# Kernel optimization log

Hardware: AMD Instinct MI355X
Metric: run time of the kernel (lower is better)

## Reference

```python
import jax, jax.numpy as jnp
import numpy as np
import math

HIDDEN = 1024
HEADS = 16
HEAD_DIM = HIDDEN // HEADS


def setup_inputs() -> dict:
    key = jax.random.key(0)
    k1, k2, k3, k4, k5 = jax.random.split(key, 5)
    B, S = 2, 2048
    scale = 1.0 / math.sqrt(HIDDEN)
    return {
        "batch_hidden": jax.random.normal(k1, (B, S, HIDDEN), dtype=jnp.float32),
        # nn.Linear weights are [out, in]; y = x @ W.T
        "Wq": jax.random.uniform(k2, (HIDDEN, HIDDEN), jnp.float32, -scale, scale),
        "Wk": jax.random.uniform(k3, (HIDDEN, HIDDEN), jnp.float32, -scale, scale),
        "Wg": jax.random.uniform(k4, (HIDDEN, HIDDEN), jnp.float32, -scale, scale),
        "bg": jax.random.uniform(k5, (HIDDEN,), jnp.float32, -scale, scale),
    }


def _split_heads(x):
    # [B,S,H] -> [B,heads,S,head_dim]
    B, S, _ = x.shape
    return x.reshape(B, S, HEADS, HEAD_DIM).transpose(0, 2, 1, 3)


def reference(batch_hidden, Wq, Wk, Wg, bg):
    # NOTE: faithful to source — value uses the KEY projection weights.
    q = batch_hidden @ Wq.T
    k = batch_hidden @ Wk.T
    v = batch_hidden @ Wk.T
    gate = jax.nn.sigmoid(batch_hidden @ Wg.T + bg)  # [B,S,H]

    q = _split_heads(q)  # [B,h,S,d]
    k = _split_heads(k)
    v = _split_heads(v)

    # source: scores = K @ Q^T (softmax over query positions)
    scores = jnp.einsum("bhkd,bhqd->bhkq", k, q) / math.sqrt(HEAD_DIM)
    attn = jax.nn.softmax(scores, axis=-1)  # [B,h,S,S]

    ctx = jnp.einsum("bhkq,bhqd->bhkd", attn, v)  # [B,h,S,d]
    ctx = ctx.transpose(0, 2, 1, 3).reshape(batch_hidden.shape)  # [B,S,H]

    out = gate * ctx
    return out, attn
```

## Files before the change

kernel.cpp:

```cpp
#include <hip/hip_runtime.h>
#include <hip/hip_bf16.h>

#define HID 1024
#define NHEADS 16
#define HDIM 64
#define SEQ 2048
#define NTOK 4096

typedef __attribute__((ext_vector_type(8))) short short8;
typedef __attribute__((ext_vector_type(4))) float f32x4;
typedef unsigned short ush;

__device__ __forceinline__ ush f2bf(float f) {
    unsigned int u = __float_as_uint(f);
    u = (u + 0x7fffu + ((u >> 16) & 1u)) >> 16;
    return (ush)u;
}
__device__ __forceinline__ void async_copy16(const void* g, void* l) {
    __builtin_amdgcn_global_load_lds(
        (const __attribute__((address_space(1))) void*)g,
        (__attribute__((address_space(3))) void*)l, 16, 0, 0);
}
#define SBAR()  __builtin_amdgcn_s_barrier()
#define SCHED() __builtin_amdgcn_sched_barrier(0)

__global__ __launch_bounds__(256) void cvt_kernel(
    const float* __restrict__ X, const float* __restrict__ Wq,
    const float* __restrict__ Wk, const float* __restrict__ Wg,
    ush* __restrict__ Xbf, ush* __restrict__ Wbf)
{
    long i = (long)blockIdx.x * 256 + threadIdx.x;
    const float* src; ush* dst; long j;
    if (i < 524288)      { src = X;  dst = Xbf;           j = i; }
    else if (i < 655360) { src = Wq; dst = Wbf;           j = i - 524288; }
    else if (i < 786432) { src = Wk; dst = Wbf + 1048576; j = i - 655360; }
    else                 { src = Wg; dst = Wbf + 2097152; j = i - 786432; }
    float4 a = *reinterpret_cast<const float4*>(src + j * 8);
    float4 b = *reinterpret_cast<const float4*>(src + j * 8 + 4);
    short8 o;
    o[0] = (short)f2bf(a.x); o[1] = (short)f2bf(a.y);
    o[2] = (short)f2bf(a.z); o[3] = (short)f2bf(a.w);
    o[4] = (short)f2bf(b.x); o[5] = (short)f2bf(b.y);
    o[6] = (short)f2bf(b.z); o[7] = (short)f2bf(b.w);
    *reinterpret_cast<short8*>(dst + j * 8) = o;
}

__global__ __launch_bounds__(256, 2) void proj_kernel(
    const ush* __restrict__ Xbf, const ush* __restrict__ Wbf,
    const float* __restrict__ bgp,
    ush* __restrict__ Qbf, ush* __restrict__ Kbf,
    float* __restrict__ gate)
{
    __shared__ __align__(16) ush As[2][128 * 64];
    __shared__ __align__(16) ush Bs[2][128 * 64];

    const int lin = blockIdx.y * 24 + blockIdx.x;
    const int swz = (lin & 7) * 96 + (lin >> 3);
    const int n0 = (swz % 24) * 128;
    const int m0 = (swz / 24) * 128;
    const int tid = threadIdx.x, lane = tid & 63, wv = tid >> 6;
    const int wm = wv >> 1, wn = wv & 1;
    const int l16 = lane & 15, lq = lane >> 4;
    const int lrow = lane >> 3, lc = lane & 7;
    const int scU = lc ^ lrow;
    const int u0 = lq ^ (l16 & 7);

    f32x4 acc[4][4];
    #pragma unroll
    for (int i = 0; i < 4; i++)
        #pragma unroll
        for (int j = 0; j < 4; j++)
            #pragma unroll
            for (int r = 0; r < 4; r++) acc[i][j][r] = 0.0f;

    const ush* gA = Xbf + (long)m0 * HID;
    const ush* gB = Wbf + (long)n0 * HID;

    auto stage = [&](int k0, int bu) {
        #pragma unroll
        for (int c = 0; c < 4; ++c) {
            int chunk = wv * 4 + c;
            int row = chunk * 8 + lrow;
            async_copy16(gA + (long)row * HID + k0 + scU * 8, &As[bu][chunk * 512]);
            async_copy16(gB + (long)row * HID + k0 + scU * 8, &Bs[bu][chunk * 512]);
        }
    };

    stage(0, 0);
    stage(64, 1);

    for (int k = 0; k < 16; ++k) {
        const int cur = k & 1;
        if (k == 15) asm volatile("s_waitcnt vmcnt(0)" ::: "memory");
        else         asm volatile("s_waitcnt vmcnt(8)" ::: "memory");
        SCHED();
        SBAR(); SCHED();
        #pragma unroll
        for (int ks = 0; ks < 2; ++ks) {
            const int uo = (ks ? (u0 ^ 4) : u0) * 8;
            short8 a[4], b[4];
            #pragma unroll
            for (int mf = 0; mf < 4; mf++)
                a[mf] = *reinterpret_cast<const short8*>(&As[cur][(wm * 64 + mf * 16 + l16) * 64 + uo]);
            #pragma unroll
            for (int nf = 0; nf < 4; nf++)
                b[nf] = *reinterpret_cast<const short8*>(&Bs[cur][(wn * 64 + nf * 16 + l16) * 64 + uo]);
            #pragma unroll
            for (int mf = 0; mf < 4; mf++)
                #pragma unroll
                for (int nf = 0; nf < 4; nf++)
                    acc[mf][nf] = __builtin_amdgcn_mfma_f32_16x16x32_bf16(a[mf], b[nf], acc[mf][nf], 0, 0, 0);
        }
        SBAR(); SCHED();
        if (k < 14) stage((k + 2) * 64, cur);
    }

    const int z = n0 >> 10;
    #pragma unroll
    for (int mf = 0; mf < 4; mf++)
        #pragma unroll
        for (int nf = 0; nf < 4; nf++) {
            int row = m0 + wm * 64 + mf * 16 + lq * 4;
            int col = (n0 + wn * 64 + nf * 16 + l16) & 1023;
            #pragma unroll
            for (int r = 0; r < 4; r++) {
                float v = acc[mf][nf][r];
                long idx = (long)(row + r) * HID + col;
                if (z == 0)      Qbf[idx] = f2bf(v * 0.18033688011112042f);
                else if (z == 1) Kbf[idx] = f2bf(v);
                else {
                    float gv = 1.0f / (1.0f + __expf(-(v + bgp[col])));
                    __builtin_nontemporal_store(gv, &gate[idx]);
                }
            }
        }
}

__global__ __launch_bounds__(256) void vt_kernel(
    const ush* __restrict__ Kbf, ush* __restrict__ VtG)
{
    __shared__ __align__(16) ush tile[64][72];
    const int s0 = blockIdx.x * 64;
    const int h  = blockIdx.y;
    const int b  = blockIdx.z;
    const int bh = b * NHEADS + h;
    const int tb = b * SEQ;
    const int colbase = h * HDIM;
    const int tid = threadIdx.x;
    #pragma unroll
    for (int i = 0; i < 2; ++i) {
        int idx = i * 256 + tid;
        int row = idx >> 3, c8 = (idx & 7) * 8;
        *reinterpret_cast<uint4*>(&tile[row][c8]) =
            *reinterpret_cast<const uint4*>(&Kbf[(long)(tb + s0 + row) * HID + colbase + c8]);
    }
    __syncthreads();
    #pragma unroll
    for (int i = 0; i < 2; ++i) {
        int idx = i * 256 + tid;
        int d = idx >> 3, c8 = (idx & 7) * 8;
        ush tmp[8];
        #pragma unroll
        for (int j = 0; j < 8; ++j) tmp[j] = tile[c8 + j][d];
        *reinterpret_cast<uint4*>(&VtG[((long)bh * HDIM + d) * SEQ + s0 + c8]) =
            *reinterpret_cast<uint4*>(tmp);
    }
}

__global__ __launch_bounds__(256, 2) void attn_kernel(
    const ush* __restrict__ Qbf,
    const ush* __restrict__ Kbf,
    const ush* __restrict__ VtG,
    float* __restrict__ outp,
    float* __restrict__ attnp)
{
    __shared__ __align__(16) ush Ks[128 * 64];
    __shared__ __align__(16) ush Qs[3][64 * 64];
    __shared__ __align__(16) ush Vt[2][64 * 64];
    __shared__ __align__(16) ush At[128][72];

    const int lin = (blockIdx.z * 16 + blockIdx.y) * 16 + blockIdx.x;
    const int swzb = (lin & 7) * 64 + (lin >> 3);
    const int kblk = swzb & 15;
    const int h    = (swzb >> 4) & 15;
    const int b    = swzb >> 8;
    const int bh   = b * NHEADS + h;
    const int tb   = b * SEQ;
    const int colbase = h * HDIM;
    const int tid  = threadIdx.x;
    const int lane = tid & 63;
    const int wv   = tid >> 6;
    const int l16  = lane & 15, lq = lane >> 4;
    const int lrow = lane >> 3, lc = lane & 7;
    const int scU  = lc ^ lrow;
    const int u0   = lq ^ (l16 & 7);

    const ush* Krow = Kbf + (long)(tb + kblk * 128) * HID + colbase;

    auto stageK = [&]() {
        #pragma unroll
        for (int c = 0; c < 4; ++c) {
            int chunk = wv * 4 + c;
            int row = chunk * 8 + lrow;
            async_copy16(Krow + (long)row * HID + scU * 8, &Ks[chunk * 512]);
        }
    };
    auto stageQ = [&](int q0, int bu) {
        #pragma unroll
        for (int c = 0; c < 2; ++c) {
            int chunk = wv * 2 + c;
            int row = chunk * 8 + lrow;
            async_copy16(Qbf + (long)(tb + q0 + row) * HID + colbase + scU * 8,
                         &Qs[bu][chunk * 512]);
        }
    };
    auto stageV = [&](int q0, int bu) {
        #pragma unroll
        for (int c = 0; c < 2; ++c) {
            int chunk = wv * 2 + c;
            int row = chunk * 8 + lrow;
            async_copy16(VtG + ((long)bh * HDIM + row) * SEQ + q0 + scU * 8,
                         &Vt[bu][chunk * 512]);
        }
    };

    stageK();
    stageQ(0, 0);
    stageQ(64, 1);

    float ps[2] = {0.0f, 0.0f};

    for (int i = 0; i < 32; ++i) {
        if (i == 31) asm volatile("s_waitcnt vmcnt(0)" ::: "memory");
        else         asm volatile("s_waitcnt vmcnt(2)" ::: "memory");
        SCHED();
        SBAR(); SCHED();
        if (i < 30) stageQ((i + 2) * 64, (i + 2) % 3);

        f32x4 acc[4][2];
        #pragma unroll
        for (int x = 0; x < 4; x++)
            #pragma unroll
            for (int y = 0; y < 2; y++)
                #pragma unroll
                for (int r = 0; r < 4; r++) acc[x][y][r] = 0.0f;

        const ush* Qb = &Qs[i % 3][0];
        #pragma unroll
        for (int ks = 0; ks < 2; ks++) {
            const int uo = (ks ? (u0 ^ 4) : u0) * 8;
            short8 aq[4], bk[2];
            #pragma unroll
            for (int mf = 0; mf < 4; mf++)
                aq[mf] = *reinterpret_cast<const short8*>(&Qb[(mf * 16 + l16) * 64 + uo]);
            #pragma unroll
            for (int nf = 0; nf < 2; nf++)
                bk[nf] = *reinterpret_cast<const short8*>(&Ks[(wv * 32 + nf * 16 + l16) * 64 + uo]);
            #pragma unroll
            for (int mf = 0; mf < 4; mf++)
                #pragma unroll
                for (int nf = 0; nf < 2; nf++)
                    acc[mf][nf] = __builtin_amdgcn_mfma_f32_16x16x32_bf16(aq[mf], bk[nf], acc[mf][nf], 0, 0, 0);
        }

        #pragma unroll
        for (int nf = 0; nf < 2; nf++) {
            float s = 0.0f;
            #pragma unroll
            for (int mf = 0; mf < 4; mf++)
                #pragma unroll
                for (int r = 0; r < 4; r++)
                    s += exp2f(acc[mf][nf][r]);
            ps[nf] += s;
        }

        SBAR(); SCHED();
    }

    float inv_r[2];
    #pragma unroll
    for (int nf = 0; nf < 2; nf++) {
        float v = ps[nf];
        v += __shfl_xor(v, 16);
        v += __shfl_xor(v, 32);
        inv_r[nf] = 1.0f / v;
    }

    f32x4 octx[2][4];
    #pragma unroll
    for (int x = 0; x < 2; x++)
        #pragma unroll
        for (int y = 0; y < 4; y++)
            #pragma unroll
            for (int r = 0; r < 4; r++) octx[x][y][r] = 0.0f;

    stageQ(0, 0); stageV(0, 0);
    stageQ(64, 1); stageV(64, 1);

    for (int i = 0; i < 32; ++i) {
        const int q0 = i << 6;
        if (i == 0)       asm volatile("s_waitcnt vmcnt(4)"  ::: "memory");
        else if (i == 1)  asm volatile("s_waitcnt vmcnt(12)" ::: "memory");
        else if (i == 31) asm volatile("s_waitcnt vmcnt(16)" ::: "memory");
        else              asm volatile("s_waitcnt vmcnt(20)" ::: "memory");
        SCHED();
        SBAR(); SCHED();
        if (i < 30) stageQ((i + 2) * 64, (i + 2) % 3);

        f32x4 acc[4][2];
        #pragma unroll
        for (int x = 0; x < 4; x++)
            #pragma unroll
            for (int y = 0; y < 2; y++)
                #pragma unroll
                for (int r = 0; r < 4; r++) acc[x][y][r] = 0.0f;

        const ush* Qb = &Qs[i % 3][0];
        #pragma unroll
        for (int ks = 0; ks < 2; ks++) {
            const int uo = (ks ? (u0 ^ 4) : u0) * 8;
            short8 aq[4], bk[2];
            #pragma unroll
            for (int mf = 0; mf < 4; mf++)
                aq[mf] = *reinterpret_cast<const short8*>(&Qb[(mf * 16 + l16) * 64 + uo]);
            #pragma unroll
            for (int nf = 0; nf < 2; nf++)
                bk[nf] = *reinterpret_cast<const short8*>(&Ks[(wv * 32 + nf * 16 + l16) * 64 + uo]);
            #pragma unroll
            for (int mf = 0; mf < 4; mf++)
                #pragma unroll
                for (int nf = 0; nf < 2; nf++)
                    acc[mf][nf] = __builtin_amdgcn_mfma_f32_16x16x32_bf16(aq[mf], bk[nf], acc[mf][nf], 0, 0, 0);
        }

        #pragma unroll
        for (int nf = 0; nf < 2; nf++) {
            const int krl = wv * 32 + nf * 16 + l16;
            const float inv = inv_r[nf];
            #pragma unroll
            for (int mf = 0; mf < 4; mf++) {
                const int qc = mf * 16 + lq * 4;
                float p0 = exp2f(acc[mf][nf][0]) * inv;
                float p1 = exp2f(acc[mf][nf][1]) * inv;
                float p2 = exp2f(acc[mf][nf][2]) * inv;
                float p3 = exp2f(acc[mf][nf][3]) * inv;
                unsigned int w0, w1;
                asm volatile("v_cvt_pk_bf16_f32 %0, %1, %2" : "=v"(w0) : "v"(p0), "v"(p1));
                asm volatile("v_cvt_pk_bf16_f32 %0, %1, %2" : "=v"(w1) : "v"(p2), "v"(p3));
                *reinterpret_cast<uint2*>(&At[krl][qc]) = make_uint2(w0, w1);
            }
        }

        asm volatile("s_waitcnt lgkmcnt(0)" ::: "memory");
        SCHED();

        uint2 wreg[8];
        const int rlo = lane >> 4;
        const int qc  = (lane & 15) * 4;
        #pragma unroll
        for (int j = 0; j < 8; ++j)
            wreg[j] = *reinterpret_cast<const uint2*>(&At[wv * 32 + j * 4 + rlo][qc]);

        #pragma unroll
        for (int ks = 0; ks < 2; ks++) {
            const int uo = (ks ? (u0 ^ 4) : u0) * 8;
            short8 a[2], bv[4];
            #pragma unroll
            for (int mf = 0; mf < 2; mf++)
                a[mf] = *reinterpret_cast<const short8*>(&At[wv * 32 + mf * 16 + l16][ks * 32 + lq * 8]);
            #pragma unroll
            for (int nf = 0; nf < 4; nf++)
                bv[nf] = *reinterpret_cast<const short8*>(&Vt[i & 1][(nf * 16 + l16) * 64 + uo]);
            #pragma unroll
            for (int mf = 0; mf < 2; mf++)
                #pragma unroll
                for (int nf = 0; nf < 4; nf++)
                    octx[mf][nf] = __builtin_amdgcn_mfma_f32_16x16x32_bf16(a[mf], bv[nf], octx[mf][nf], 0, 0, 0);
        }

        SBAR(); SCHED();
        if (i < 30) stageV((i + 2) * 64, i & 1);

        #pragma unroll
        for (int j = 0; j < 8; ++j) {
            const int rl = wv * 32 + j * 4 + rlo;
            f32x4 st;
            st[0] = __uint_as_float(wreg[j].x << 16);
            st[1] = __uint_as_float(wreg[j].x & 0xffff0000u);
            st[2] = __uint_as_float(wreg[j].y << 16);
            st[3] = __uint_as_float(wreg[j].y & 0xffff0000u);
            __builtin_nontemporal_store(st,
                reinterpret_cast<f32x4*>(attnp + ((long)bh * SEQ + kblk * 128 + rl) * SEQ + q0 + qc));
        }
    }

    #pragma unroll
    for (int mf = 0; mf < 2; mf++)
        #pragma unroll
        for (int nf = 0; nf < 4; nf++) {
            int row = tb + kblk * 128 + wv * 32 + mf * 16 + lq * 4;
            int col = colbase + nf * 16 + l16;
            #pragma unroll
            for (int r = 0; r < 4; r++) {
                long idx = (long)(row + r) * HID + col;
                float g = __builtin_nontemporal_load(&outp[idx]);
                __builtin_nontemporal_store(g * octx[mf][nf][r], &outp[idx]);
            }
        }
}

extern "C" void kernel_launch(void* const* d_in, const int* in_sizes, int n_in,
                              void* d_out, int out_size, void* d_ws, size_t ws_size,
                              hipStream_t stream)
{
    const float* X  = (const float*)d_in[0];
    const float* Wq = (const float*)d_in[1];
    const float* Wk = (const float*)d_in[2];
    const float* Wg = (const float*)d_in[3];
    const float* bg = (const float*)d_in[4];

    float* outp  = (float*)d_out;
    float* attnp = outp + (long)NTOK * HID;

    ush* Qbf = (ush*)d_ws;
    ush* Kbf = Qbf + (long)NTOK * HID;
    ush* VtG = Kbf + (long)NTOK * HID;

    ush* Xbf = (ush*)(outp + 134742016L);
    ush* Wbf = Xbf + (long)NTOK * HID;

    cvt_kernel<<<3584, 256, 0, stream>>>(X, Wq, Wk, Wg, Xbf, Wbf);
    proj_kernel<<<dim3(24, 32), 256, 0, stream>>>(Xbf, Wbf, bg, Qbf, Kbf, outp);
    vt_kernel<<<dim3(32, 16, 2), 256, 0, stream>>>(Kbf, VtG);
    attn_kernel<<<dim3(16, 16, 2), 256, 0, stream>>>(Qbf, Kbf, VtG, outp, attnp);
}
```

Baseline: 223.5 us.

## Fuse V-transpose into projection epilogue and quad-buffer Q in pass one

The projection kernel now writes the transposed K (used as V) directly from its accumulators with packed bf16 conversions, removing the separate vt_kernel launch and its extra read of K. In the attention kernel's first pass, Q staging moves from triple to quad buffering (the fourth slot aliases the At scratch area), which lets the end-of-iteration barrier be dropped. The transposed stores are 8-byte strided writes, so they may be less coalesced than the old LDS-based transpose.

```diff
diff --git a/kernel.cpp b/kernel.cpp
--- a/kernel.cpp
+++ b/kernel.cpp
@@ -49,6 +49,7 @@
     const ush* __restrict__ Xbf, const ush* __restrict__ Wbf,
     const float* __restrict__ bgp,
     ush* __restrict__ Qbf, ush* __restrict__ Kbf,
+    ush* __restrict__ VtG,
     float* __restrict__ gate)
 {
     __shared__ __align__(16) ush As[2][128 * 64];
@@ -121,7 +122,8 @@
         #pragma unroll
         for (int nf = 0; nf < 4; nf++) {
             int row = m0 + wm * 64 + mf * 16 + lq * 4;
-            int col = (n0 + wn * 64 + nf * 16 + l16) & 1023;
+            int gcol = n0 + wn * 64 + nf * 16 + l16;
+            int col = gcol & 1023;
             #pragma unroll
             for (int r = 0; r < 4; r++) {
                 float v = acc[mf][nf][r];
@@ -133,38 +135,19 @@
                     __builtin_nontemporal_store(gv, &gate[idx]);
                 }
             }
-        }
-}
-
-__global__ __launch_bounds__(256) void vt_kernel(
-    const ush* __restrict__ Kbf, ush* __restrict__ VtG)
-{
-    __shared__ __align__(16) ush tile[64][72];
-    const int s0 = blockIdx.x * 64;
-    const int h  = blockIdx.y;
-    const int b  = blockIdx.z;
-    const int bh = b * NHEADS + h;
-    const int tb = b * SEQ;
-    const int colbase = h * HDIM;
-    const int tid = threadIdx.x;
-    #pragma unroll
-    for (int i = 0; i < 2; ++i) {
-        int idx = i * 256 + tid;
-        int row = idx >> 3, c8 = (idx & 7) * 8;
-        *reinterpret_cast<uint4*>(&tile[row][c8]) =
-            *reinterpret_cast<const uint4*>(&Kbf[(long)(tb + s0 + row) * HID + colbase + c8]);
-    }
-    __syncthreads();
-    #pragma unroll
-    for (int i = 0; i < 2; ++i) {
-        int idx = i * 256 + tid;
-        int d = idx >> 3, c8 = (idx & 7) * 8;
-        ush tmp[8];
-        #pragma unroll
-        for (int j = 0; j < 8; ++j) tmp[j] = tile[c8 + j][d];
-        *reinterpret_cast<uint4*>(&VtG[((long)bh * HDIM + d) * SEQ + s0 + c8]) =
-            *reinterpret_cast<uint4*>(tmp);
-    }
+            if (z == 1) {
+                int bb = row >> 11, s = row & 2047;
+                int bh = bb * NHEADS + (col >> 6);
+                int d  = col & 63;
+                unsigned int w0, w1;
+                asm volatile("v_cvt_pk_bf16_f32 %0, %1, %2" : "=v"(w0)
+                             : "v"(acc[mf][nf][0]), "v"(acc[mf][nf][1]));
+                asm volatile("v_cvt_pk_bf16_f32 %0, %1, %2" : "=v"(w1)
+                             : "v"(acc[mf][nf][2]), "v"(acc[mf][nf][3]));
+                *reinterpret_cast<uint2*>(&VtG[((long)bh * HDIM + d) * SEQ + s]) =
+                    make_uint2(w0, w1);
+            }
+        }
 }
 
 __global__ __launch_bounds__(256, 2) void attn_kernel(
@@ -175,9 +158,10 @@
     float* __restrict__ attnp)
 {
     __shared__ __align__(16) ush Ks[128 * 64];
-    __shared__ __align__(16) ush Qs[3][64 * 64];
+    __shared__ __align__(16) ush QsA[3 * 4096 + 128 * 72];
     __shared__ __align__(16) ush Vt[2][64 * 64];
-    __shared__ __align__(16) ush At[128][72];
+
+    ush (*At)[72] = reinterpret_cast<ush(*)[72]>(&QsA[12288]);
 
     const int lin = (blockIdx.z * 16 + blockIdx.y) * 16 + blockIdx.x;
     const int swzb = (lin & 7) * 64 + (lin >> 3);
@@ -211,7 +195,7 @@
             int chunk = wv * 2 + c;
             int row = chunk * 8 + lrow;
             async_copy16(Qbf + (long)(tb + q0 + row) * HID + colbase + scU * 8,
-                         &Qs[bu][chunk * 512]);
+                         &QsA[bu * 4096 + chunk * 512]);
         }
     };
     auto stageV = [&](int q0, int bu) {
@@ -231,11 +215,11 @@
     float ps[2] = {0.0f, 0.0f};
 
     for (int i = 0; i < 32; ++i) {
-        if (i == 31) asm volatile("s_waitcnt vmcnt(0)" ::: "memory");
+        if (i >= 30) asm volatile("s_waitcnt vmcnt(0)" ::: "memory");
         else         asm volatile("s_waitcnt vmcnt(2)" ::: "memory");
         SCHED();
         SBAR(); SCHED();
-        if (i < 30) stageQ((i + 2) * 64, (i + 2) % 3);
+        if (i < 30) stageQ((i + 2) * 64, (i + 2) & 3);
 
         f32x4 acc[4][2];
         #pragma unroll
@@ -245,7 +229,7 @@
                 #pragma unroll
                 for (int r = 0; r < 4; r++) acc[x][y][r] = 0.0f;
 
-        const ush* Qb = &Qs[i % 3][0];
+        const ush* Qb = &QsA[(i & 3) * 4096];
         #pragma unroll
         for (int ks = 0; ks < 2; ks++) {
             const int uo = (ks ? (u0 ^ 4) : u0) * 8;
@@ -273,8 +257,6 @@
                     s += exp2f(acc[mf][nf][r]);
             ps[nf] += s;
         }
-
-        SBAR(); SCHED();
     }
 
     float inv_r[2];
@@ -294,6 +276,7 @@
             #pragma unroll
             for (int r = 0; r < 4; r++) octx[x][y][r] = 0.0f;
 
+    SBAR();
     stageQ(0, 0); stageV(0, 0);
     stageQ(64, 1); stageV(64, 1);
 
@@ -315,7 +298,7 @@
                 #pragma unroll
                 for (int r = 0; r < 4; r++) acc[x][y][r] = 0.0f;
 
-        const ush* Qb = &Qs[i % 3][0];
+        const ush* Qb = &QsA[(i % 3) * 4096];
         #pragma unroll
         for (int ks = 0; ks < 2; ks++) {
             const int uo = (ks ? (u0 ^ 4) : u0) * 8;
@@ -430,7 +413,6 @@
     ush* Wbf = Xbf + (long)NTOK * HID;
 
     cvt_kernel<<<3584, 256, 0, stream>>>(X, Wq, Wk, Wg, Xbf, Wbf);
-    proj_kernel<<<dim3(24, 32), 256, 0, stream>>>(Xbf, Wbf, bg, Qbf, Kbf, outp);
-    vt_kernel<<<dim3(32, 16, 2), 256, 0, stream>>>(Kbf, VtG);
+    proj_kernel<<<dim3(24, 32), 256, 0, stream>>>(Xbf, Wbf, bg, Qbf, Kbf, VtG, outp);
     attn_kernel<<<dim3(16, 16, 2), 256, 0, stream>>>(Qbf, Kbf, VtG, outp, attnp);
 }
```

New measurement: 219.3 us. About the same (-1.8%).
